# Optimization experiments

Measured on AMD Instinct MI355X. Metric: run time of the kernel, lower is better.

The kernel has to match this reference:

```python
import jax, jax.numpy as jnp
import numpy as np

EPS = 1e-5  # torch layer_norm / group_norm default eps

def _ln(x, w):
    mu = x.mean(-1, keepdims=True)
    var = x.var(-1, keepdims=True)
    return (x - mu) / jnp.sqrt(var + EPS) * w

def _mh_ln(x, w, nh):
    # MultiHeadLayerNorm == group_norm with nh groups over last dim, weight, no bias
    B, S, D = x.shape
    xh = x.reshape(B, S, nh, D // nh)
    mu = xh.mean(-1, keepdims=True)
    var = xh.var(-1, keepdims=True)
    return ((xh - mu) / jnp.sqrt(var + EPS)).reshape(B, S, D) * w

def _causal_conv(x, k, b):
    # depthwise causal conv1d, x: (B,S,C), k: (C,K)
    K = k.shape[1]
    S = x.shape[1]
    xp = jnp.pad(x, ((0, 0), (K - 1, 0), (0, 0)))
    y = sum(xp[:, i:i + S, :] * k[:, i] for i in range(K))
    return y + b

def _headwise(x, W):
    # LinearHeadwiseExpand: block-diagonal linear, W: (nh, out_per_head, in_per_head)
    B, S, D = x.shape
    nh, o, i = W.shape
    xh = x.reshape(B, S, nh, i)
    return jnp.einsum('bshi,hoi->bsho', xh, W).reshape(B, S, nh * o)

def _mlstm_parallel(q, k, v, ig, fg, eps=1e-6):
    # q,k,v: (B,NH,S,DH); ig,fg: (B,NH,S) gate preactivations
    B, NH, S, DH = q.shape
    logf = jax.nn.log_sigmoid(fg)
    lc = jnp.cumsum(logf, axis=-1)
    # log_fg_matrix[t,s] = sum_{j=s+1..t} log sigmoid(f_j)
    lfm = lc[..., :, None] - lc[..., None, :]
    mask = jnp.tril(jnp.ones((S, S), dtype=bool))
    logD = jnp.where(mask, lfm + ig[..., None, :], -jnp.inf)
    maxD = jnp.max(logD, axis=-1, keepdims=True)
    D = jnp.exp(logD - maxD)
    qk = jnp.einsum('bhsd,bhtd->bhst', q, k) / jnp.sqrt(jnp.float32(DH))
    C = qk * D
    normalizer = jnp.maximum(jnp.abs(C.sum(-1, keepdims=True)), jnp.exp(-maxD))
    return jnp.einsum('bhst,bhtd->bhsd', C / (normalizer + eps), v)

def _slstm_scan(gx, R, b):
    # gx: (B,S,NH,4,DH) input-gate preacts (i,f,z,o); R: (NH,DH,4,DH); b: (NH,4,DH)
    B, S, NH, G, DH = gx.shape
    gx_t = jnp.moveaxis(gx, 1, 0)
    z0 = jnp.zeros((B, NH, DH), gx.dtype)
    def step(carry, inp):
        y, c, n, m = carry
        g, t = inp
        raw = g + jnp.einsum('bhd,hdge->bhge', y, R) + b
        iraw, fraw, zraw, oraw = raw[:, :, 0], raw[:, :, 1], raw[:, :, 2], raw[:, :, 3]
        logfplusm = m + jax.nn.log_sigmoid(fraw)
        mnew = jnp.where(t == 0, iraw, jnp.maximum(iraw, logfplusm))
        og = jax.nn.sigmoid(oraw)
        ig = jnp.exp(iraw - mnew)
        fg = jnp.exp(logfplusm - mnew)
        cnew = fg * c + ig * jnp.tanh(zraw)
        nnew = fg * n + ig
        ynew = og * cnew / nnew
        return (ynew, cnew, nnew, mnew), ynew
    _, ys = jax.lax.scan(step, (z0, z0, z0, z0), (gx_t, jnp.arange(S)))
    return jnp.moveaxis(ys, 0, 1)  # (B,S,NH,DH)

def _forward(x, W_in, b_in, ln0_w, m_Wup, m_bup, m_convk, m_convb, m_Wq, m_bq, m_Wk, m_bk, m_Wv, m_bv, m_Wig, m_big, m_Wfg, m_bfg, m_onw, m_skip, m_Wd, m_bd, ln1_w, s_convk, s_convb, s_Wi, s_Wf, s_Wz, s_Wo, s_R, s_b, s_gnw, ffn_nw, f_Wu, f_bu, f_Wd, f_bd, post_w, fc_W, fc_b):
    B, S, _ = x.shape
    NH, DH = 4, 64  # mLSTM heads
    h = x @ W_in.T + b_in  # input_proj (dropout is identity in eval)
    # ---- block 0: mLSTM (pre-norm residual) ----
    r = _ln(h, ln0_w)
    up = r @ m_Wup.T + m_bup
    xm, z = jnp.split(up, 2, axis=-1)  # (B,S,256) each
    xc = jax.nn.silu(_causal_conv(xm, m_convk, m_convb))
    q = _headwise(xc, m_Wq) + m_bq
    k = _headwise(xc, m_Wk) + m_bk
    v = _headwise(xm, m_Wv) + m_bv
    qkv = jnp.concatenate([q, k, v], axis=-1)  # (B,S,768)
    igp = (qkv @ m_Wig.T + m_big).transpose(0, 2, 1)  # (B,NH,S)
    fgp = (qkv @ m_Wfg.T + m_bfg).transpose(0, 2, 1)
    qh = q.reshape(B, S, NH, DH).transpose(0, 2, 1, 3)
    kh = k.reshape(B, S, NH, DH).transpose(0, 2, 1, 3)
    vh = v.reshape(B, S, NH, DH).transpose(0, 2, 1, 3)
    hc = _mlstm_parallel(qh, kh, vh, igp, fgp)
    hc = hc.transpose(0, 2, 1, 3).reshape(B, S, NH * DH)
    ht = _mh_ln(hc, m_onw, NH)
    hs = (ht + m_skip * xc) * jax.nn.silu(z)
    h = h + hs @ m_Wd.T + m_bd
    # ---- block 1: sLSTM (pre-norm residual) ----
    SNH, SDH = 4, 32
    r = _ln(h, ln1_w)
    rc = jax.nn.silu(_causal_conv(r, s_convk, s_convb))
    gi = _headwise(rc, s_Wi).reshape(B, S, SNH, SDH)
    gf = _headwise(rc, s_Wf).reshape(B, S, SNH, SDH)
    gz = _headwise(r, s_Wz).reshape(B, S, SNH, SDH)
    go = _headwise(r, s_Wo).reshape(B, S, SNH, SDH)
    gx = jnp.stack([gi, gf, gz, go], axis=3)  # (B,S,NH,4,DH)
    ys = _slstm_scan(gx, s_R, s_b).reshape(B, S, SNH * SDH)
    h = h + _mh_ln(ys, s_gnw, SNH)
    # gated feedforward (gelu)
    r = _ln(h, ffn_nw)
    u = r @ f_Wu.T + f_bu
    g, u2 = jnp.split(u, 2, axis=-1)
    h = h + (jax.nn.gelu(g, approximate=False) * u2) @ f_Wd.T + f_bd
    hp = _ln(h, post_w)
    return hp[:, -1, :] @ fc_W.T + fc_b

def setup_inputs() -> dict:
    key = jax.random.key(0)
    ks = iter(jax.random.split(key, 64))
    def rn(shape, scale=1.0):
        return jax.random.normal(next(ks), shape, dtype=jnp.float32) * scale
    B, S, F, D = 8, 1024, 75, 128
    inner = 256
    return dict(
        x=rn((B, S, F)),
        W_in=rn((D, F), F ** -0.5), b_in=rn((D,), 0.02),
        ln0_w=jnp.ones((D,), jnp.float32),
        m_Wup=rn((2 * inner, D), D ** -0.5), m_bup=rn((2 * inner,), 0.02),
        m_convk=rn((inner, 4), 0.5), m_convb=rn((inner,), 0.02),
        m_Wq=rn((64, 4, 4), 0.5), m_bq=rn((inner,), 0.02),
        m_Wk=rn((64, 4, 4), 0.5), m_bk=rn((inner,), 0.02),
        m_Wv=rn((64, 4, 4), 0.5), m_bv=rn((inner,), 0.02),
        m_Wig=rn((4, 3 * inner), (3 * inner) ** -0.5), m_big=rn((4,), 0.1),
        m_Wfg=rn((4, 3 * inner), (3 * inner) ** -0.5), m_bfg=rn((4,), 0.1) + 3.0,
        m_onw=jnp.ones((inner,), jnp.float32),
        m_skip=jnp.ones((inner,), jnp.float32),
        m_Wd=rn((D, inner), inner ** -0.5), m_bd=rn((D,), 0.02),
        ln1_w=jnp.ones((D,), jnp.float32),
        s_convk=rn((D, 4), 0.5), s_convb=rn((D,), 0.02),
        s_Wi=rn((4, 32, 32), 32 ** -0.5),
        s_Wf=rn((4, 32, 32), 32 ** -0.5),
        s_Wz=rn((4, 32, 32), 32 ** -0.5),
        s_Wo=rn((4, 32, 32), 32 ** -0.5),
        s_R=rn((4, 32, 4, 32), 32 ** -0.5),
        s_b=rn((4, 4, 32), 0.1),
        s_gnw=jnp.ones((D,), jnp.float32),
        ffn_nw=jnp.ones((D,), jnp.float32),
        f_Wu=rn((384, D), D ** -0.5), f_bu=rn((384,), 0.02),
        f_Wd=rn((D, 192), 192 ** -0.5), f_bd=rn((D,), 0.02),
        post_w=jnp.ones((D,), jnp.float32),
        fc_W=rn((1, D), D ** -0.5), fc_b=rn((1,), 0.02),
    )

def reference(x, W_in, b_in, ln0_w, m_Wup, m_bup, m_convk, m_convb, m_Wq, m_bq, m_Wk, m_bk, m_Wv, m_bv, m_Wig, m_big, m_Wfg, m_bfg, m_onw, m_skip, m_Wd, m_bd, ln1_w, s_convk, s_convb, s_Wi, s_Wf, s_Wz, s_Wo, s_R, s_b, s_gnw, ffn_nw, f_Wu, f_bu, f_Wd, f_bd, post_w, fc_W, fc_b):
    return _forward(x, W_in, b_in, ln0_w, m_Wup, m_bup, m_convk, m_convb, m_Wq, m_bq, m_Wk, m_bk, m_Wv, m_bv, m_Wig, m_big, m_Wfg, m_bfg, m_onw, m_skip, m_Wd, m_bd, ln1_w, s_convk, s_convb, s_Wi, s_Wf, s_Wz, s_Wo, s_R, s_b, s_gnw, ffn_nw, f_Wu, f_bu, f_Wd, f_bd, post_w, fc_W, fc_b)
```

## Files before the change

kernel.cpp:

```cpp
#include <hip/hip_runtime.h>
#include <hip/hip_bf16.h>
#include <math.h>

#define B_ 8
#define S_ 1024
#define F_ 75
#define D_ 128
#define INNER_ 256
#define NH_ 4
#define DH_ 64
#define MROWS_ (B_*S_)

static __device__ __forceinline__ float frcp(float x){ return __builtin_amdgcn_rcpf(x); }
static __device__ __forceinline__ float fsigm(float x){ return frcp(1.0f + __expf(-x)); }
static __device__ __forceinline__ float flogsig(float x){
    return fminf(x, 0.f) - __logf(1.0f + __expf(-fabsf(x)));
}
static __device__ __forceinline__ float ftanh(float z){
    return 1.0f - 2.0f*frcp(__expf(2.0f*z) + 1.0f);
}

__global__ __launch_bounds__(256, 2) void gemm_bias_big(
        const float* __restrict__ A, const float* __restrict__ W,
        const float* __restrict__ bias, const float* __restrict__ res,
        float* __restrict__ C, int M, int N, int K) {
    __shared__ float As[64*68];
    __shared__ float Ws[64*68];
    int tid = threadIdx.x;
    int wid = tid >> 6, lane = tid & 63;
    int wy = wid >> 1, wx = wid & 1;
    int sg = lane >> 3, tg = lane & 7;
    int m0 = blockIdx.y*64, n0 = blockIdx.x*64;
    int r = tid >> 2, c0 = (tid & 3) << 4;
    bool vec = ((K & 3) == 0);
    float acc[4][4];
    #pragma unroll
    for (int i = 0; i < 4; ++i)
        #pragma unroll
        for (int j = 0; j < 4; ++j) acc[i][j] = 0.f;

    for (int k0 = 0; k0 < K; k0 += 64) {
        __syncthreads();
        const float* Ar = A + (size_t)(m0+r)*K + k0;
        const float* Wr = W + (size_t)(n0+r)*K + k0;
        if (vec) {
            #pragma unroll
            for (int i = 0; i < 4; ++i) {
                *(float4*)(&As[r*68 + c0 + 4*i]) = *(const float4*)(Ar + c0 + 4*i);
                *(float4*)(&Ws[r*68 + c0 + 4*i]) = *(const float4*)(Wr + c0 + 4*i);
            }
        } else {
            #pragma unroll
            for (int i = 0; i < 4; ++i)
                #pragma unroll
                for (int e = 0; e < 4; ++e) {
                    int c = c0 + 4*i + e;
                    bool ok = (k0 + c) < K;
                    As[r*68 + c] = ok ? Ar[c] : 0.f;
                    Ws[r*68 + c] = ok ? Wr[c] : 0.f;
                }
        }
        __syncthreads();
        const float* arow = &As[(32*wy + sg)*68];
        const float* brow = &Ws[(32*wx + tg)*68];
        #pragma unroll 2
        for (int d = 0; d < 64; d += 4) {
            float4 b0 = *(const float4*)(brow + 0*544 + d);
            float4 b1 = *(const float4*)(brow + 1*544 + d);
            float4 b2 = *(const float4*)(brow + 2*544 + d);
            float4 b3 = *(const float4*)(brow + 3*544 + d);
            #pragma unroll
            for (int i = 0; i < 4; ++i) {
                float4 a = *(const float4*)(arow + i*544 + d);
                acc[i][0] += a.x*b0.x + a.y*b0.y + a.z*b0.z + a.w*b0.w;
                acc[i][1] += a.x*b1.x + a.y*b1.y + a.z*b1.z + a.w*b1.w;
                acc[i][2] += a.x*b2.x + a.y*b2.y + a.z*b2.z + a.w*b2.w;
                acc[i][3] += a.x*b3.x + a.y*b3.y + a.z*b3.z + a.w*b3.w;
            }
        }
    }
    #pragma unroll
    for (int i = 0; i < 4; ++i) {
        int m = m0 + 32*wy + 8*i + sg;
        #pragma unroll
        for (int j = 0; j < 4; ++j) {
            int n = n0 + 32*wx + 8*j + tg;
            float v = acc[i][j] + bias[n];
            if (res) v += res[(size_t)m*N + n];
            C[(size_t)m*N + n] = v;
        }
    }
}

__global__ void ln_kernel(const float* __restrict__ X, const float* __restrict__ w,
                          float* __restrict__ Y) {
    int row = blockIdx.x, t = threadIdx.x;
    float v = X[(size_t)row*128 + t];
    __shared__ float s1[128], s2[128];
    s1[t]=v; s2[t]=v*v; __syncthreads();
    for (int off=64; off>0; off>>=1){
        if (t<off){ s1[t]+=s1[t+off]; s2[t]+=s2[t+off]; }
        __syncthreads();
    }
    float mu = s1[0]*(1.f/128.f);
    float var = s2[0]*(1.f/128.f) - mu*mu;
    Y[(size_t)row*128 + t] = (v-mu)*rsqrtf(var+1e-5f)*w[t];
}

__global__ void conv_silu(const float* __restrict__ X, int ldx,
                          const float* __restrict__ kw, const float* __restrict__ kb,
                          float* __restrict__ Y, int ldy, int C) {
    int idx = blockIdx.x*blockDim.x + threadIdx.x;
    int total = MROWS_*C;
    if (idx >= total) return;
    int c = idx % C; int bs = idx / C;
    int s = bs % S_; int b = bs / S_;
    float acc = kb[c];
    #pragma unroll
    for (int i = 0; i < 4; ++i) {
        int sp = s - 3 + i;
        if (sp >= 0) acc += X[((size_t)b*S_+sp)*ldx + c] * kw[c*4+i];
    }
    Y[((size_t)b*S_+s)*ldy + c] = acc * fsigm(acc);
}

__global__ void headwise4(const float* __restrict__ X, int ldx,
                          const float* __restrict__ W, const float* __restrict__ bias,
                          float* __restrict__ Y) {
    int idx = blockIdx.x*blockDim.x + threadIdx.x;
    int total = MROWS_*INNER_;
    if (idx >= total) return;
    int co = idx % INNER_; int bs = idx / INNER_;
    int h = co >> 2, o = co & 3;
    const float* Wh = W + ((size_t)h*4 + o)*4;
    const float* xr = X + (size_t)bs*ldx + h*4;
    float acc = bias[co];
    #pragma unroll
    for (int i = 0; i < 4; ++i) acc += xr[i]*Wh[i];
    Y[(size_t)bs*INNER_ + co] = acc;
}

__global__ void slstm_gates(const float* __restrict__ rc, const float* __restrict__ r,
                            const float* __restrict__ Wi, const float* __restrict__ Wf,
                            const float* __restrict__ Wz, const float* __restrict__ Wo,
                            float* __restrict__ GX) {
    int idx = blockIdx.x*blockDim.x + threadIdx.x;
    int total = MROWS_*128;
    if (idx >= total) return;
    int co = idx % 128; int bs = idx / 128;
    int h = co >> 5, o = co & 31;
    size_t wb = ((size_t)h*32 + o)*32;
    const float* xc_ = rc + (size_t)bs*128 + h*32;
    const float* xr_ = r  + (size_t)bs*128 + h*32;
    float di=0.f, df=0.f, dz=0.f, doo=0.f;
    #pragma unroll
    for (int i = 0; i < 32; ++i) {
        float a = xc_[i], c = xr_[i];
        di  += a*Wi[wb+i];
        df  += a*Wf[wb+i];
        dz  += c*Wz[wb+i];
        doo += c*Wo[wb+i];
    }
    float* g = GX + (size_t)bs*512 + h*128 + o;
    g[0]  = di;
    g[32] = df;
    g[64] = dz;
    g[96] = doo;
}

__global__ void gateproj(const float* __restrict__ q, const float* __restrict__ k,
                         const float* __restrict__ v,
                         const float* __restrict__ Wig, const float* __restrict__ big,
                         const float* __restrict__ Wfg, const float* __restrict__ bfg,
                         float* __restrict__ igp, float* __restrict__ fgp) {
    int bs = blockIdx.x; int lane = threadIdx.x;
    int b = bs / S_, s = bs % S_;
    const float* qr = q + (size_t)bs*INNER_;
    const float* kr = k + (size_t)bs*INNER_;
    const float* vr = v + (size_t)bs*INNER_;
    float dots[8];
    #pragma unroll
    for (int g=0; g<8; ++g) dots[g]=0.f;
    for (int c = lane; c < INNER_; c += 64) {
        float qv = qr[c], kv = kr[c], vv = vr[c];
        #pragma unroll
        for (int g=0; g<4; ++g) {
            dots[g]   += qv*Wig[g*768+c] + kv*Wig[g*768+256+c] + vv*Wig[g*768+512+c];
            dots[4+g] += qv*Wfg[g*768+c] + kv*Wfg[g*768+256+c] + vv*Wfg[g*768+512+c];
        }
    }
    #pragma unroll
    for (int off=32; off>0; off>>=1)
        #pragma unroll
        for (int g=0; g<8; ++g) dots[g] += __shfl_down(dots[g], off, 64);
    if (lane == 0) {
        #pragma unroll
        for (int g=0; g<4; ++g) {
            igp[((size_t)b*NH_+g)*S_ + s] = dots[g]   + big[g];
            fgp[((size_t)b*NH_+g)*S_ + s] = dots[4+g] + bfg[g];
        }
    }
}

__global__ void mlstm_scan_pre(const float* __restrict__ igp, const float* __restrict__ fgp,
                               float* __restrict__ lc, float* __restrict__ av,
                               float* __restrict__ mx) {
    int bh = blockIdx.x; int t = threadIdx.x;
    __shared__ float buf[2][1024];
    float ls = flogsig(fgp[(size_t)bh*S_ + t]);
    int cur = 0;
    buf[0][t] = ls; __syncthreads();
    for (int off=1; off<1024; off<<=1) {
        float x2 = buf[cur][t];
        if (t >= off) x2 += buf[cur][t-off];
        buf[cur^1][t] = x2; cur ^= 1; __syncthreads();
    }
    float lcv = buf[cur][t];
    lc[(size_t)bh*S_+t] = lcv;
    float a = igp[(size_t)bh*S_+t] - lcv;
    av[(size_t)bh*S_+t] = a;
    __syncthreads();
    cur = 0; buf[0][t] = a; __syncthreads();
    for (int off=1; off<1024; off<<=1) {
        float x2 = buf[cur][t];
        if (t >= off) x2 = fmaxf(x2, buf[cur][t-off]);
        buf[cur^1][t] = x2; cur ^= 1; __syncthreads();
    }
    mx[(size_t)bh*S_+t] = buf[cur][t];
}

__global__ __launch_bounds__(256, 2) void mlstm_attn_tiled(
        const float* __restrict__ q, const float* __restrict__ k,
        const float* __restrict__ v, const float* __restrict__ lc,
        const float* __restrict__ av, const float* __restrict__ mx,
        float* __restrict__ hc) {
    int bid = blockIdx.x;
    int stile = 15 - (bid & 15);
    int bh = bid >> 4;
    int hh = bh & 3, b = bh >> 2;
    int s0 = stile << 6;
    int tid = threadIdx.x;
    int wid = tid >> 6, lane = tid & 63;
    int wy = wid >> 1, wx = wid & 1;
    int sg = lane >> 3, tg = lane & 7;

    __shared__ float qs[64*68];
    __shared__ float kst[64*68];
    __shared__ float vtT[64*68];
    __shared__ float avt[64], maxsL[64], normL[64], rsumL[128];

    const size_t bhS = (size_t)bh * S_;
    {
        int r = tid >> 2, c0 = (tid & 3) << 4;
        const float* qg = q + ((size_t)(b*S_) + s0 + r)*INNER_ + hh*64;
        #pragma unroll
        for (int i = 0; i < 4; ++i) {
            float4 t4 = *(const float4*)(qg + c0 + 4*i);
            float4 w4; w4.x=t4.x*0.125f; w4.y=t4.y*0.125f; w4.z=t4.z*0.125f; w4.w=t4.w*0.125f;
            *(float4*)(&qs[r*68 + c0 + 4*i]) = w4;
        }
        if (tid < 64) maxsL[tid] = lc[bhS + s0 + tid] + mx[bhS + s0 + tid];
    }
    float msv[4];
    #pragma unroll
    for (int i = 0; i < 4; ++i)
        msv[i] = mx[bhS + s0 + 32*wy + 8*i + sg];

    float O[4][4];
    float rsAcc[4];
    #pragma unroll
    for (int i = 0; i < 4; ++i) {
        rsAcc[i] = 0.f;
        #pragma unroll
        for (int j = 0; j < 4; ++j) O[i][j] = 0.f;
    }

    for (int t0 = 0; t0 <= s0; t0 += 64) {
        __syncthreads();
        {
            int r = tid >> 2, c0 = (tid & 3) << 4;
            const float* kg = k + ((size_t)(b*S_) + t0 + r)*INNER_ + hh*64;
            const float* vg = v + ((size_t)(b*S_) + t0 + r)*INNER_ + hh*64;
            #pragma unroll
            for (int i = 0; i < 4; ++i) {
                *(float4*)(&kst[r*68 + c0 + 4*i]) = *(const float4*)(kg + c0 + 4*i);
                float4 v4 = *(const float4*)(vg + c0 + 4*i);
                int dc = c0 + 4*i;
                vtT[(dc+0)*68 + r] = v4.x;
                vtT[(dc+1)*68 + r] = v4.y;
                vtT[(dc+2)*68 + r] = v4.z;
                vtT[(dc+3)*68 + r] = v4.w;
            }
            if (tid < 64) avt[tid] = av[bhS + t0 + tid];
        }
        __syncthreads();
        float dot[4][4];
        #pragma unroll
        for (int i = 0; i < 4; ++i)
            #pragma unroll
            for (int j = 0; j < 4; ++j) dot[i][j] = 0.f;
        {
            const float* qrow = &qs[(32*wy + sg)*68];
            const float* krow = &kst[(32*wx + tg)*68];
            #pragma unroll 2
            for (int d = 0; d < 64; d += 4) {
                float4 b0 = *(const float4*)(krow + 0*544 + d);
                float4 b1 = *(const float4*)(krow + 1*544 + d);
                float4 b2 = *(const float4*)(krow + 2*544 + d);
                float4 b3 = *(const float4*)(krow + 3*544 + d);
                #pragma unroll
                for (int i = 0; i < 4; ++i) {
                    float4 a = *(const float4*)(qrow + i*544 + d);
                    dot[i][0] += a.x*b0.x + a.y*b0.y + a.z*b0.z + a.w*b0.w;
                    dot[i][1] += a.x*b1.x + a.y*b1.y + a.z*b1.z + a.w*b1.w;
                    dot[i][2] += a.x*b2.x + a.y*b2.y + a.z*b2.z + a.w*b2.w;
                    dot[i][3] += a.x*b3.x + a.y*b3.y + a.z*b3.z + a.w*b3.w;
                }
            }
        }
        __syncthreads();
        #pragma unroll
        for (int i = 0; i < 4; ++i) {
            int s_loc = 32*wy + 8*i + sg;
            float rp = 0.f;
            #pragma unroll
            for (int j = 0; j < 4; ++j) {
                int t_loc = 32*wx + 8*j + tg;
                bool ok = (t0 + t_loc) <= (s0 + s_loc);
                float p = ok ? dot[i][j]*__expf(avt[t_loc] - msv[i]) : 0.f;
                kst[s_loc*68 + t_loc] = p;
                rp += p;
            }
            rp += __shfl_xor(rp, 1);
            rp += __shfl_xor(rp, 2);
            rp += __shfl_xor(rp, 4);
            rsAcc[i] += rp;
        }
        __syncthreads();
        {
            const float* prow = &kst[(32*wy + sg)*68];
            const float* vrow = &vtT[(32*wx + tg)*68];
            #pragma unroll 2
            for (int tt = 0; tt < 64; tt += 4) {
                float4 b0 = *(const float4*)(vrow + 0*544 + tt);
                float4 b1 = *(const float4*)(vrow + 1*544 + tt);
                float4 b2 = *(const float4*)(vrow + 2*544 + tt);
                float4 b3 = *(const float4*)(vrow + 3*544 + tt);
                #pragma unroll
                for (int i = 0; i < 4; ++i) {
                    float4 a = *(const float4*)(prow + i*544 + tt);
                    O[i][0] += a.x*b0.x + a.y*b0.y + a.z*b0.z + a.w*b0.w;
                    O[i][1] += a.x*b1.x + a.y*b1.y + a.z*b1.z + a.w*b1.w;
                    O[i][2] += a.x*b2.x + a.y*b2.y + a.z*b2.z + a.w*b2.w;
                    O[i][3] += a.x*b3.x + a.y*b3.y + a.z*b3.z + a.w*b3.w;
                }
            }
        }
    }
    if (tg == 0) {
        #pragma unroll
        for (int i = 0; i < 4; ++i)
            rsumL[wx*64 + 32*wy + 8*i + sg] = rsAcc[i];
    }
    __syncthreads();
    if (tid < 64) {
        float tot = rsumL[tid] + rsumL[64 + tid];
        normL[tid] = fmaxf(fabsf(tot), __expf(-maxsL[tid])) + 1e-6f;
    }
    __syncthreads();
    #pragma unroll
    for (int i = 0; i < 4; ++i) {
        int s_loc = 32*wy + 8*i + sg;
        float inv = 1.0f / normL[s_loc];
        #pragma unroll
        for (int j = 0; j < 4; ++j) {
            int d_loc = 32*wx + 8*j + tg;
            hc[((size_t)(b*S_) + s0 + s_loc)*INNER_ + hh*64 + d_loc] = O[i][j] * inv;
        }
    }
}

__global__ void mlstm_out(const float* __restrict__ hc, const float* __restrict__ xc,
                          const float* __restrict__ up, const float* __restrict__ onw,
                          const float* __restrict__ skip, float* __restrict__ hs) {
    int row = blockIdx.x; int c = threadIdx.x;
    float v = hc[(size_t)row*INNER_ + c];
    __shared__ float s1[256], s2[256];
    s1[c]=v; s2[c]=v*v; __syncthreads();
    int li = c & 63;
    for (int off=32; off>0; off>>=1){
        if (li < off){ s1[c]+=s1[c+off]; s2[c]+=s2[c+off]; }
        __syncthreads();
    }
    int base = c & ~63;
    float mu = s1[base]*(1.f/64.f);
    float var = s2[base]*(1.f/64.f) - mu*mu;
    float ht = (v-mu)*rsqrtf(var+1e-5f)*onw[c];
    float z = up[(size_t)row*512 + 256 + c];
    hs[(size_t)row*INNER_ + c] = (ht + skip[c]*xc[(size_t)row*INNER_+c]) * (z*fsigm(z));
}

__global__ __launch_bounds__(64, 1) void slstm_scan_wave(
        const float* __restrict__ gx, const float* __restrict__ R,
        const float* __restrict__ bb, float* __restrict__ ys) {
    int blk = blockIdx.x; int hh = blk & 3; int b = blk >> 2;
    int l = threadIdx.x;
    int e = l >> 1, p = l & 1;
    int o0 = p*32 + e, o1 = (p+2)*32 + e;
    float Rc0[32], Rc1[32];
    #pragma unroll
    for (int d = 0; d < 32; ++d) {
        Rc0[d] = R[(size_t)(hh*32 + d)*128 + o0];
        Rc1[d] = R[(size_t)(hh*32 + d)*128 + o1];
        asm volatile("" : "+v"(Rc0[d]));
        asm volatile("" : "+v"(Rc1[d]));
    }
    float bj0 = bb[hh*128 + o0], bj1 = bb[hh*128 + o1];
    float cst = 0.f, nst = 0.f, mst = 0.f, y = 0.f;
    const float* gbase = gx + (size_t)(b*S_)*512 + hh*128;
    float* ybase = ys + (size_t)(b*S_)*128 + hh*32 + e;
    float ga[4], gb[4];
    #pragma unroll
    for (int u = 0; u < 4; ++u) {
        ga[u] = gbase[(size_t)u*512 + o0];
        gb[u] = gbase[(size_t)u*512 + o1];
    }
    for (int t = 0; t < S_; t += 4) {
        float gna[4], gnb[4];
        #pragma unroll
        for (int u = 0; u < 4; ++u) {
            int tn = t + 4 + u;
            size_t off = (size_t)(tn < S_ ? tn : 0) * 512;
            gna[u] = gbase[off + o0];
            gnb[u] = gbase[off + o1];
        }
        #pragma unroll
        for (int u = 0; u < 4; ++u) {
            float a0=0.f, a1=0.f, a2=0.f, a3=0.f;
            float c0=0.f, c1=0.f, c2=0.f, c3=0.f;
            #pragma unroll
            for (int d = 0; d < 32; d += 4) {
                float y0 = __int_as_float(__builtin_amdgcn_readlane(__float_as_int(y), 2*d));
                float y1 = __int_as_float(__builtin_amdgcn_readlane(__float_as_int(y), 2*d+2));
                float y2 = __int_as_float(__builtin_amdgcn_readlane(__float_as_int(y), 2*d+4));
                float y3 = __int_as_float(__builtin_amdgcn_readlane(__float_as_int(y), 2*d+6));
                a0 += y0*Rc0[d];   c0 += y0*Rc1[d];
                a1 += y1*Rc0[d+1]; c1 += y1*Rc1[d+1];
                a2 += y2*Rc0[d+2]; c2 += y2*Rc1[d+2];
                a3 += y3*Rc0[d+3]; c3 += y3*Rc1[d+3];
            }
            float r0 = ga[u] + bj0 + ((a0+a1)+(a2+a3));
            float r1 = gb[u] + bj1 + ((c0+c1)+(c2+c3));
            float fo0 = __int_as_float(__builtin_amdgcn_mov_dpp(__float_as_int(r0), 0xB1, 0xF, 0xF, true));
            float fo1 = __int_as_float(__builtin_amdgcn_mov_dpp(__float_as_int(r1), 0xB1, 0xF, 0xF, true));
            float iraw = p ? fo0 : r0;
            float fraw = p ? r0 : fo0;
            float zraw = p ? fo1 : r1;
            float oraw = p ? r1 : fo1;
            int t_abs = t + u;
            float lfm = mst + flogsig(fraw);
            float mnew = (t_abs == 0) ? iraw : fmaxf(iraw, lfm);
            float igv = __expf(iraw - mnew), fgv = __expf(lfm - mnew);
            cst = fgv*cst + igv*ftanh(zraw);
            nst = fgv*nst + igv;
            mst = mnew;
            y = cst * frcp(nst * (1.0f + __expf(-oraw)));
            if (p == 0) ybase[(size_t)t_abs*128] = y;
        }
        #pragma unroll
        for (int u = 0; u < 4; ++u) { ga[u] = gna[u]; gb[u] = gnb[u]; }
    }
}

__global__ void slstm_addnorm(const float* __restrict__ ys, const float* __restrict__ w,
                              float* __restrict__ h) {
    int row = blockIdx.x; int c = threadIdx.x;
    float v = ys[(size_t)row*128 + c];
    __shared__ float s1[128], s2[128];
    s1[c]=v; s2[c]=v*v; __syncthreads();
    int li = c & 31;
    for (int off=16; off>0; off>>=1){
        if (li < off){ s1[c]+=s1[c+off]; s2[c]+=s2[c+off]; }
        __syncthreads();
    }
    int base = c & ~31;
    float mu = s1[base]*(1.f/32.f);
    float var = s2[base]*(1.f/32.f) - mu*mu;
    h[(size_t)row*128 + c] += (v-mu)*rsqrtf(var+1e-5f)*w[c];
}

__global__ void ffn_act(const float* __restrict__ u, float* __restrict__ act) {
    int idx = blockIdx.x*blockDim.x + threadIdx.x;
    int total = MROWS_*192;
    if (idx >= total) return;
    int j = idx % 192; int m = idx / 192;
    float g  = u[(size_t)m*384 + j];
    float u2 = u[(size_t)m*384 + 192 + j];
    float ge = 0.5f*g*(1.0f + erff(g*0.70710678118f));
    act[(size_t)m*192 + j] = ge*u2;
}

__global__ void final_fc(const float* __restrict__ hp, const float* __restrict__ fcW,
                         const float* __restrict__ fcb, float* __restrict__ out) {
    int b = blockIdx.x; int lane = threadIdx.x;
    const float* r = hp + ((size_t)b*S_ + (S_-1))*128;
    float acc = r[lane]*fcW[lane] + r[lane+64]*fcW[lane+64];
    #pragma unroll
    for (int off=32; off>0; off>>=1) acc += __shfl_down(acc, off, 64);
    if (lane == 0) out[b] = acc + fcb[0];
}

extern "C" void kernel_launch(void* const* d_in, const int* in_sizes, int n_in,
                              void* d_out, int out_size, void* d_ws, size_t ws_size,
                              hipStream_t stream) {
    const float* x       = (const float*)d_in[0];
    const float* W_in    = (const float*)d_in[1];
    const float* b_in    = (const float*)d_in[2];
    const float* ln0_w   = (const float*)d_in[3];
    const float* m_Wup   = (const float*)d_in[4];
    const float* m_bup   = (const float*)d_in[5];
    const float* m_convk = (const float*)d_in[6];
    const float* m_convb = (const float*)d_in[7];
    const float* m_Wq    = (const float*)d_in[8];
    const float* m_bq    = (const float*)d_in[9];
    const float* m_Wk    = (const float*)d_in[10];
    const float* m_bk    = (const float*)d_in[11];
    const float* m_Wv    = (const float*)d_in[12];
    const float* m_bv    = (const float*)d_in[13];
    const float* m_Wig   = (const float*)d_in[14];
    const float* m_big   = (const float*)d_in[15];
    const float* m_Wfg   = (const float*)d_in[16];
    const float* m_bfg   = (const float*)d_in[17];
    const float* m_onw   = (const float*)d_in[18];
    const float* m_skip  = (const float*)d_in[19];
    const float* m_Wd    = (const float*)d_in[20];
    const float* m_bd    = (const float*)d_in[21];
    const float* ln1_w   = (const float*)d_in[22];
    const float* s_convk = (const float*)d_in[23];
    const float* s_convb = (const float*)d_in[24];
    const float* s_Wi    = (const float*)d_in[25];
    const float* s_Wf    = (const float*)d_in[26];
    const float* s_Wz    = (const float*)d_in[27];
    const float* s_Wo    = (const float*)d_in[28];
    const float* s_R     = (const float*)d_in[29];
    const float* s_b     = (const float*)d_in[30];
    const float* s_gnw   = (const float*)d_in[31];
    const float* ffn_nw  = (const float*)d_in[32];
    const float* f_Wu    = (const float*)d_in[33];
    const float* f_bu    = (const float*)d_in[34];
    const float* f_Wd    = (const float*)d_in[35];
    const float* f_bd    = (const float*)d_in[36];
    const float* post_w  = (const float*)d_in[37];
    const float* fc_W    = (const float*)d_in[38];
    const float* fc_b    = (const float*)d_in[39];
    float* out = (float*)d_out;

    float* W = (float*)d_ws;
    const size_t M1 = 1048576;
    float* h    = W;
    float* r    = W + 1*M1;
    float* up   = W + 2*M1;
    float* xc   = W + 6*M1;
    float* q    = W + 8*M1;
    float* kbuf = W + 10*M1;
    float* vbuf = W + 12*M1;
    float* hc   = W + 14*M1;
    float* igp  = W + 16*M1;
    float* fgp  = igp + 32768;
    float* lc   = fgp + 32768;
    float* av   = lc  + 32768;
    float* mx   = av  + 32768;
    float* hs   = q;
    float* gx   = kbuf;
    float* ys   = hc;
    float* rc   = xc;
    float* u    = up;
    float* act  = q;
    float* hp   = r;

    gemm_bias_big<<<dim3(128/64, MROWS_/64), 256, 0, stream>>>(x, W_in, b_in, nullptr, h, MROWS_, 128, F_);
    ln_kernel<<<MROWS_, 128, 0, stream>>>(h, ln0_w, r);
    gemm_bias_big<<<dim3(512/64, MROWS_/64), 256, 0, stream>>>(r, m_Wup, m_bup, nullptr, up, MROWS_, 512, 128);
    conv_silu<<<(MROWS_*256)/256, 256, 0, stream>>>(up, 512, m_convk, m_convb, xc, 256, 256);
    headwise4<<<(MROWS_*256)/256, 256, 0, stream>>>(xc, 256, m_Wq, m_bq, q);
    headwise4<<<(MROWS_*256)/256, 256, 0, stream>>>(xc, 256, m_Wk, m_bk, kbuf);
    headwise4<<<(MROWS_*256)/256, 256, 0, stream>>>(up, 512, m_Wv, m_bv, vbuf);
    gateproj<<<MROWS_, 64, 0, stream>>>(q, kbuf, vbuf, m_Wig, m_big, m_Wfg, m_bfg, igp, fgp);
    mlstm_scan_pre<<<B_*NH_, 1024, 0, stream>>>(igp, fgp, lc, av, mx);
    mlstm_attn_tiled<<<B_*NH_*16, 256, 0, stream>>>(q, kbuf, vbuf, lc, av, mx, hc);
    mlstm_out<<<MROWS_, 256, 0, stream>>>(hc, xc, up, m_onw, m_skip, hs);
    gemm_bias_big<<<dim3(128/64, MROWS_/64), 256, 0, stream>>>(hs, m_Wd, m_bd, h, h, MROWS_, 128, 256);
    ln_kernel<<<MROWS_, 128, 0, stream>>>(h, ln1_w, r);
    conv_silu<<<(MROWS_*128)/256, 256, 0, stream>>>(r, 128, s_convk, s_convb, rc, 128, 128);
    slstm_gates<<<(MROWS_*128)/256, 256, 0, stream>>>(rc, r, s_Wi, s_Wf, s_Wz, s_Wo, gx);
    slstm_scan_wave<<<B_*NH_, 64, 0, stream>>>(gx, s_R, s_b, ys);
    slstm_addnorm<<<MROWS_, 128, 0, stream>>>(ys, s_gnw, h);
    ln_kernel<<<MROWS_, 128, 0, stream>>>(h, ffn_nw, r);
    gemm_bias_big<<<dim3(384/64, MROWS_/64), 256, 0, stream>>>(r, f_Wu, f_bu, nullptr, u, MROWS_, 384, 128);
    ffn_act<<<(MROWS_*192)/256, 256, 0, stream>>>(u, act);
    gemm_bias_big<<<dim3(128/64, MROWS_/64), 256, 0, stream>>>(act, f_Wd, f_bd, h, h, MROWS_, 128, 192);
    ln_kernel<<<MROWS_, 128, 0, stream>>>(h, post_w, hp);
    final_fc<<<B_, 64, 0, stream>>>(hp, fc_W, fc_b, out);
    (void)in_sizes; (void)n_in; (void)out_size; (void)ws_size;
}
```

Before: 957.5 us.

## Fuse mLSTM conv/qkv/gate kernels, sLSTM conv/gates, addnorm+LN, and final LN+FC

Merges the mLSTM conv+SiLU, three headwise projections and the gate projection into one per-row kernel that keeps intermediates in registers. It also fuses the sLSTM conv with the gate projection through shared memory, fuses the group-norm residual add with the following FFN layer norm, and replaces the full post layer norm with one applied only to the last timestep inside the final FC. The aim is to cut kernel launches and repeated global-memory round trips for intermediates. The price is 64-thread blocks with heavier per-thread work in the mLSTM kernel.

```diff
diff --git a/kernel.cpp b/kernel.cpp
--- a/kernel.cpp
+++ b/kernel.cpp
@@ -107,99 +107,118 @@
     Y[(size_t)row*128 + t] = (v-mu)*rsqrtf(var+1e-5f)*w[t];
 }
 
-__global__ void conv_silu(const float* __restrict__ X, int ldx,
-                          const float* __restrict__ kw, const float* __restrict__ kb,
-                          float* __restrict__ Y, int ldy, int C) {
-    int idx = blockIdx.x*blockDim.x + threadIdx.x;
-    int total = MROWS_*C;
-    if (idx >= total) return;
-    int c = idx % C; int bs = idx / C;
-    int s = bs % S_; int b = bs / S_;
-    float acc = kb[c];
+__global__ __launch_bounds__(64) void mlstm_qkv(
+        const float* __restrict__ up, const float* __restrict__ convk,
+        const float* __restrict__ convb,
+        const float* __restrict__ Wq, const float* __restrict__ bq,
+        const float* __restrict__ Wk, const float* __restrict__ bk,
+        const float* __restrict__ Wv, const float* __restrict__ bv,
+        const float* __restrict__ Wig, const float* __restrict__ big,
+        const float* __restrict__ Wfg, const float* __restrict__ bfg,
+        float* __restrict__ xc, float* __restrict__ q, float* __restrict__ k,
+        float* __restrict__ v, float* __restrict__ igp, float* __restrict__ fgp) {
+    int row = blockIdx.x;
+    int b = row >> 10, s = row & 1023;
+    int l = threadIdx.x;
+    int c0 = l*4;
+    float4 xm[4];
     #pragma unroll
     for (int i = 0; i < 4; ++i) {
         int sp = s - 3 + i;
-        if (sp >= 0) acc += X[((size_t)b*S_+sp)*ldx + c] * kw[c*4+i];
-    }
-    Y[((size_t)b*S_+s)*ldy + c] = acc * fsigm(acc);
-}
-
-__global__ void headwise4(const float* __restrict__ X, int ldx,
-                          const float* __restrict__ W, const float* __restrict__ bias,
-                          float* __restrict__ Y) {
-    int idx = blockIdx.x*blockDim.x + threadIdx.x;
-    int total = MROWS_*INNER_;
-    if (idx >= total) return;
-    int co = idx % INNER_; int bs = idx / INNER_;
-    int h = co >> 2, o = co & 3;
-    const float* Wh = W + ((size_t)h*4 + o)*4;
-    const float* xr = X + (size_t)bs*ldx + h*4;
-    float acc = bias[co];
-    #pragma unroll
-    for (int i = 0; i < 4; ++i) acc += xr[i]*Wh[i];
-    Y[(size_t)bs*INNER_ + co] = acc;
-}
-
-__global__ void slstm_gates(const float* __restrict__ rc, const float* __restrict__ r,
-                            const float* __restrict__ Wi, const float* __restrict__ Wf,
-                            const float* __restrict__ Wz, const float* __restrict__ Wo,
-                            float* __restrict__ GX) {
-    int idx = blockIdx.x*blockDim.x + threadIdx.x;
-    int total = MROWS_*128;
-    if (idx >= total) return;
-    int co = idx % 128; int bs = idx / 128;
-    int h = co >> 5, o = co & 31;
+        if (sp >= 0) xm[i] = *(const float4*)(up + (size_t)(row-3+i)*512 + c0);
+        else         xm[i] = make_float4(0.f,0.f,0.f,0.f);
+    }
+    float xcv[4];
+    #pragma unroll
+    for (int j = 0; j < 4; ++j) {
+        int c = c0 + j;
+        float acc = convb[c];
+        #pragma unroll
+        for (int i = 0; i < 4; ++i)
+            acc += ((const float*)&xm[i])[j] * convk[c*4+i];
+        xcv[j] = acc * fsigm(acc);
+    }
+    *(float4*)(xc + (size_t)row*256 + c0) = make_float4(xcv[0],xcv[1],xcv[2],xcv[3]);
+    float qv[4], kv[4], vv[4];
+    #pragma unroll
+    for (int o = 0; o < 4; ++o) {
+        const float* wq = Wq + ((size_t)l*4 + o)*4;
+        const float* wk = Wk + ((size_t)l*4 + o)*4;
+        const float* wv = Wv + ((size_t)l*4 + o)*4;
+        float aq = bq[c0+o], ak = bk[c0+o], avv = bv[c0+o];
+        #pragma unroll
+        for (int i = 0; i < 4; ++i) {
+            aq  += xcv[i]*wq[i];
+            ak  += xcv[i]*wk[i];
+            avv += ((const float*)&xm[3])[i]*wv[i];
+        }
+        qv[o]=aq; kv[o]=ak; vv[o]=avv;
+    }
+    *(float4*)(q + (size_t)row*256 + c0) = make_float4(qv[0],qv[1],qv[2],qv[3]);
+    *(float4*)(k + (size_t)row*256 + c0) = make_float4(kv[0],kv[1],kv[2],kv[3]);
+    *(float4*)(v + (size_t)row*256 + c0) = make_float4(vv[0],vv[1],vv[2],vv[3]);
+    float dots[8];
+    #pragma unroll
+    for (int g = 0; g < 4; ++g) {
+        float di = 0.f, df = 0.f;
+        #pragma unroll
+        for (int j = 0; j < 4; ++j) {
+            di += qv[j]*Wig[g*768 + c0 + j] + kv[j]*Wig[g*768 + 256 + c0 + j]
+                + vv[j]*Wig[g*768 + 512 + c0 + j];
+            df += qv[j]*Wfg[g*768 + c0 + j] + kv[j]*Wfg[g*768 + 256 + c0 + j]
+                + vv[j]*Wfg[g*768 + 512 + c0 + j];
+        }
+        dots[g] = di; dots[4+g] = df;
+    }
+    #pragma unroll
+    for (int off = 32; off > 0; off >>= 1)
+        #pragma unroll
+        for (int g = 0; g < 8; ++g) dots[g] += __shfl_down(dots[g], off, 64);
+    if (l == 0) {
+        #pragma unroll
+        for (int g = 0; g < 4; ++g) {
+            igp[((size_t)b*NH_+g)*S_ + s] = dots[g]   + big[g];
+            fgp[((size_t)b*NH_+g)*S_ + s] = dots[4+g] + bfg[g];
+        }
+    }
+}
+
+__global__ __launch_bounds__(128) void slstm_convgates(
+        const float* __restrict__ r, const float* __restrict__ convk,
+        const float* __restrict__ convb, const float* __restrict__ Wi,
+        const float* __restrict__ Wf, const float* __restrict__ Wz,
+        const float* __restrict__ Wo, float* __restrict__ GX) {
+    int row = blockIdx.x; int s = row & 1023;
+    int c = threadIdx.x;
+    __shared__ float rcL[128], rL[128];
+    float rv = r[(size_t)row*128 + c];
+    float acc = convb[c];
+    #pragma unroll
+    for (int i = 0; i < 4; ++i) {
+        int sp = s - 3 + i;
+        if (sp >= 0) acc += r[(size_t)(row-3+i)*128 + c]*convk[c*4+i];
+    }
+    float rcv = acc * fsigm(acc);
+    rcL[c] = rcv; rL[c] = rv;
+    __syncthreads();
+    int h = c >> 5, o = c & 31;
     size_t wb = ((size_t)h*32 + o)*32;
-    const float* xc_ = rc + (size_t)bs*128 + h*32;
-    const float* xr_ = r  + (size_t)bs*128 + h*32;
+    const float* rc_ = rcL + h*32;
+    const float* rr_ = rL + h*32;
     float di=0.f, df=0.f, dz=0.f, doo=0.f;
     #pragma unroll
     for (int i = 0; i < 32; ++i) {
-        float a = xc_[i], c = xr_[i];
+        float a = rc_[i], cc = rr_[i];
         di  += a*Wi[wb+i];
         df  += a*Wf[wb+i];
-        dz  += c*Wz[wb+i];
-        doo += c*Wo[wb+i];
-    }
-    float* g = GX + (size_t)bs*512 + h*128 + o;
+        dz  += cc*Wz[wb+i];
+        doo += cc*Wo[wb+i];
+    }
+    float* g = GX + (size_t)row*512 + h*128 + o;
     g[0]  = di;
     g[32] = df;
     g[64] = dz;
     g[96] = doo;
-}
-
-__global__ void gateproj(const float* __restrict__ q, const float* __restrict__ k,
-                         const float* __restrict__ v,
-                         const float* __restrict__ Wig, const float* __restrict__ big,
-                         const float* __restrict__ Wfg, const float* __restrict__ bfg,
-                         float* __restrict__ igp, float* __restrict__ fgp) {
-    int bs = blockIdx.x; int lane = threadIdx.x;
-    int b = bs / S_, s = bs % S_;
-    const float* qr = q + (size_t)bs*INNER_;
-    const float* kr = k + (size_t)bs*INNER_;
-    const float* vr = v + (size_t)bs*INNER_;
-    float dots[8];
-    #pragma unroll
-    for (int g=0; g<8; ++g) dots[g]=0.f;
-    for (int c = lane; c < INNER_; c += 64) {
-        float qv = qr[c], kv = kr[c], vv = vr[c];
-        #pragma unroll
-        for (int g=0; g<4; ++g) {
-            dots[g]   += qv*Wig[g*768+c] + kv*Wig[g*768+256+c] + vv*Wig[g*768+512+c];
-            dots[4+g] += qv*Wfg[g*768+c] + kv*Wfg[g*768+256+c] + vv*Wfg[g*768+512+c];
-        }
-    }
-    #pragma unroll
-    for (int off=32; off>0; off>>=1)
-        #pragma unroll
-        for (int g=0; g<8; ++g) dots[g] += __shfl_down(dots[g], off, 64);
-    if (lane == 0) {
-        #pragma unroll
-        for (int g=0; g<4; ++g) {
-            igp[((size_t)b*NH_+g)*S_ + s] = dots[g]   + big[g];
-            fgp[((size_t)b*NH_+g)*S_ + s] = dots[4+g] + bfg[g];
-        }
-    }
 }
 
 __global__ void mlstm_scan_pre(const float* __restrict__ igp, const float* __restrict__ fgp,
@@ -472,11 +491,12 @@
     }
 }
 
-__global__ void slstm_addnorm(const float* __restrict__ ys, const float* __restrict__ w,
-                              float* __restrict__ h) {
+__global__ void slstm_addnorm_ln(const float* __restrict__ ys, const float* __restrict__ gnw,
+                                 const float* __restrict__ ffnw,
+                                 float* __restrict__ h, float* __restrict__ r) {
     int row = blockIdx.x; int c = threadIdx.x;
+    __shared__ float s1[128], s2[128];
     float v = ys[(size_t)row*128 + c];
-    __shared__ float s1[128], s2[128];
     s1[c]=v; s2[c]=v*v; __syncthreads();
     int li = c & 31;
     for (int off=16; off>0; off>>=1){
@@ -486,7 +506,17 @@
     int base = c & ~31;
     float mu = s1[base]*(1.f/32.f);
     float var = s2[base]*(1.f/32.f) - mu*mu;
-    h[(size_t)row*128 + c] += (v-mu)*rsqrtf(var+1e-5f)*w[c];
+    float hn = h[(size_t)row*128 + c] + (v-mu)*rsqrtf(var+1e-5f)*gnw[c];
+    h[(size_t)row*128 + c] = hn;
+    __syncthreads();
+    s1[c]=hn; s2[c]=hn*hn; __syncthreads();
+    for (int off=64; off>0; off>>=1){
+        if (c<off){ s1[c]+=s1[c+off]; s2[c]+=s2[c+off]; }
+        __syncthreads();
+    }
+    float mu2 = s1[0]*(1.f/128.f);
+    float var2 = s2[0]*(1.f/128.f) - mu2*mu2;
+    r[(size_t)row*128 + c] = (hn-mu2)*rsqrtf(var2+1e-5f)*ffnw[c];
 }
 
 __global__ void ffn_act(const float* __restrict__ u, float* __restrict__ act) {
@@ -500,14 +530,28 @@
     act[(size_t)m*192 + j] = ge*u2;
 }
 
-__global__ void final_fc(const float* __restrict__ hp, const float* __restrict__ fcW,
-                         const float* __restrict__ fcb, float* __restrict__ out) {
-    int b = blockIdx.x; int lane = threadIdx.x;
-    const float* r = hp + ((size_t)b*S_ + (S_-1))*128;
-    float acc = r[lane]*fcW[lane] + r[lane+64]*fcW[lane+64];
-    #pragma unroll
-    for (int off=32; off>0; off>>=1) acc += __shfl_down(acc, off, 64);
-    if (lane == 0) out[b] = acc + fcb[0];
+__global__ void final_ln_fc(const float* __restrict__ h, const float* __restrict__ postw,
+                            const float* __restrict__ fcW, const float* __restrict__ fcb,
+                            float* __restrict__ out) {
+    int b = blockIdx.x; int t = threadIdx.x;
+    const float* hr = h + (size_t)(b*S_ + S_-1)*128;
+    float v = hr[t];
+    __shared__ float s1[128], s2[128];
+    s1[t]=v; s2[t]=v*v; __syncthreads();
+    for (int off=64; off>0; off>>=1){
+        if (t<off){ s1[t]+=s1[t+off]; s2[t]+=s2[t+off]; }
+        __syncthreads();
+    }
+    float mu = s1[0]*(1.f/128.f);
+    float var = s2[0]*(1.f/128.f) - mu*mu;
+    float hp = (v-mu)*rsqrtf(var+1e-5f)*postw[t];
+    __syncthreads();
+    s1[t] = hp*fcW[t]; __syncthreads();
+    for (int off=64; off>0; off>>=1){
+        if (t<off) s1[t]+=s1[t+off];
+        __syncthreads();
+    }
+    if (t == 0) out[b] = s1[0] + fcb[0];
 }
 
 extern "C" void kernel_launch(void* const* d_in, const int* in_sizes, int n_in,
@@ -573,33 +617,26 @@
     float* hs   = q;
     float* gx   = kbuf;
     float* ys   = hc;
-    float* rc   = xc;
     float* u    = up;
     float* act  = q;
-    float* hp   = r;
 
     gemm_bias_big<<<dim3(128/64, MROWS_/64), 256, 0, stream>>>(x, W_in, b_in, nullptr, h, MROWS_, 128, F_);
     ln_kernel<<<MROWS_, 128, 0, stream>>>(h, ln0_w, r);
     gemm_bias_big<<<dim3(512/64, MROWS_/64), 256, 0, stream>>>(r, m_Wup, m_bup, nullptr, up, MROWS_, 512, 128);
-    conv_silu<<<(MROWS_*256)/256, 256, 0, stream>>>(up, 512, m_convk, m_convb, xc, 256, 256);
-    headwise4<<<(MROWS_*256)/256, 256, 0, stream>>>(xc, 256, m_Wq, m_bq, q);
-    headwise4<<<(MROWS_*256)/256, 256, 0, stream>>>(xc, 256, m_Wk, m_bk, kbuf);
-    headwise4<<<(MROWS_*256)/256, 256, 0, stream>>>(up, 512, m_Wv, m_bv, vbuf);
-    gateproj<<<MROWS_, 64, 0, stream>>>(q, kbuf, vbuf, m_Wig, m_big, m_Wfg, m_bfg, igp, fgp);
+    mlstm_qkv<<<MROWS_, 64, 0, stream>>>(up, m_convk, m_convb, m_Wq, m_bq, m_Wk, m_bk,
+                                         m_Wv, m_bv, m_Wig, m_big, m_Wfg, m_bfg,
+                                         xc, q, kbuf, vbuf, igp, fgp);
     mlstm_scan_pre<<<B_*NH_, 1024, 0, stream>>>(igp, fgp, lc, av, mx);
     mlstm_attn_tiled<<<B_*NH_*16, 256, 0, stream>>>(q, kbuf, vbuf, lc, av, mx, hc);
     mlstm_out<<<MROWS_, 256, 0, stream>>>(hc, xc, up, m_onw, m_skip, hs);
     gemm_bias_big<<<dim3(128/64, MROWS_/64), 256, 0, stream>>>(hs, m_Wd, m_bd, h, h, MROWS_, 128, 256);
     ln_kernel<<<MROWS_, 128, 0, stream>>>(h, ln1_w, r);
-    conv_silu<<<(MROWS_*128)/256, 256, 0, stream>>>(r, 128, s_convk, s_convb, rc, 128, 128);
-    slstm_gates<<<(MROWS_*128)/256, 256, 0, stream>>>(rc, r, s_Wi, s_Wf, s_Wz, s_Wo, gx);
+    slstm_convgates<<<MROWS_, 128, 0, stream>>>(r, s_convk, s_convb, s_Wi, s_Wf, s_Wz, s_Wo, gx);
     slstm_scan_wave<<<B_*NH_, 64, 0, stream>>>(gx, s_R, s_b, ys);
-    slstm_addnorm<<<MROWS_, 128, 0, stream>>>(ys, s_gnw, h);
-    ln_kernel<<<MROWS_, 128, 0, stream>>>(h, ffn_nw, r);
+    slstm_addnorm_ln<<<MROWS_, 128, 0, stream>>>(ys, s_gnw, ffn_nw, h, r);
     gemm_bias_big<<<dim3(384/64, MROWS_/64), 256, 0, stream>>>(r, f_Wu, f_bu, nullptr, u, MROWS_, 384, 128);
     ffn_act<<<(MROWS_*192)/256, 256, 0, stream>>>(u, act);
     gemm_bias_big<<<dim3(128/64, MROWS_/64), 256, 0, stream>>>(act, f_Wd, f_bd, h, h, MROWS_, 128, 192);
-    ln_kernel<<<MROWS_, 128, 0, stream>>>(h, post_w, hp);
-    final_fc<<<B_, 64, 0, stream>>>(hp, fc_W, fc_b, out);
+    final_ln_fc<<<B_, 128, 0, stream>>>(h, post_w, fc_W, fc_b, out);
     (void)in_sizes; (void)n_in; (void)out_size; (void)ws_size;
 }
```

Result: faster. 915.6 us (-4.4%).
